# Performance work log

Measured on AMD Instinct MI355X. Metric: run time of the kernel, lower is better.

## Reference

```python
import jax, jax.numpy as jnp
import numpy as np

N_HEAD = 16
ROPE_BASE = 10000.0

def rotate_half(x):
    half = x.shape[-1] // 2
    return jnp.concatenate((-x[..., half:], x[..., :half]), axis=-1)

def rope_freqs(T, head_dim, dtype):
    inv_freq = 1.0 / (ROPE_BASE ** (jnp.arange(0, head_dim, 2, dtype=jnp.float32) / head_dim))
    t = jnp.arange(T, dtype=jnp.float32)
    freqs = t[:, None] * inv_freq[None, :]          # [T, head_dim//2]
    emb = jnp.concatenate((freqs, freqs), axis=-1)  # [T, head_dim]
    return emb.astype(dtype)

def setup_inputs() -> dict:
    key = jax.random.key(0)
    ks = jax.random.split(key, 9)
    B, T, C = 2, 2048, 1024
    s = 1.0 / np.sqrt(C)
    return {
        'x':  jax.random.normal(ks[0], (B, T, C), jnp.float32),
        'Wq': jax.random.normal(ks[1], (C, C), jnp.float32) * s,
        'bq': jnp.zeros((C,), jnp.float32),
        'Wk': jax.random.normal(ks[2], (C, C), jnp.float32) * s,
        'bk': jnp.zeros((C,), jnp.float32),
        'Wv': jax.random.normal(ks[3], (C, C), jnp.float32) * s,
        'bv': jnp.zeros((C,), jnp.float32),
        'Wp': jax.random.normal(ks[4], (C, C), jnp.float32) * s,
        'bp': jnp.zeros((C,), jnp.float32),
    }

def reference(x, Wq, bq, Wk, bk, Wv, bv, Wp, bp):
    B, T, C = x.shape
    H = N_HEAD
    D = C // H
    # torch Linear: y = x @ W.T + b
    def heads(y):
        return y.reshape(B, T, H, D).transpose(0, 2, 1, 3)  # [B,H,T,D]
    q = heads(x @ Wq.T + bq)
    k = heads(x @ Wk.T + bk)
    v = heads(x @ Wv.T + bv)
    # inline RoPE
    emb = rope_freqs(T, D, x.dtype)          # [T, D]
    cos, sin = jnp.cos(emb), jnp.sin(emb)
    q = q * cos + rotate_half(q) * sin
    k = k * cos + rotate_half(k) * sin
    # full T x T scores with causal masked softmax
    att = jnp.einsum('bhtd,bhsd->bhts', q, k) * (1.0 / jnp.sqrt(jnp.array(D, x.dtype)))
    causal = jnp.tril(jnp.ones((T, T), bool))
    att = jnp.where(causal[None, None], att, jnp.array(-jnp.inf, att.dtype))
    att = jax.nn.softmax(att, axis=-1)
    y = jnp.einsum('bhts,bhsd->bhtd', att, v)  # [B,H,T,D]
    y = y.transpose(0, 2, 1, 3).reshape(B, T, C)
    return y @ Wp.T + bp
```

## Files before the change

kernel.cpp:

```cpp
#include <hip/hip_runtime.h>
#include <hip/hip_bf16.h>
#include <stdint.h>

typedef unsigned short u16;
typedef __attribute__((ext_vector_type(8))) short bf16x8;
typedef __attribute__((ext_vector_type(4))) float f32x4;
typedef __attribute__((ext_vector_type(2))) unsigned int u32x2;

typedef const __attribute__((address_space(1))) unsigned int* gu32p;
typedef __attribute__((address_space(3))) unsigned int* lu32p;

__device__ __forceinline__ void gl_lds16(const u16* g, u16* l) {
  __builtin_amdgcn_global_load_lds((gu32p)(const void*)g, (lu32p)(void*)l, 16, 0, 0);
}

__device__ __forceinline__ u16 f2bf(float f) {
  union { float f; unsigned u; } v; v.f = f;
  unsigned r = v.u + 0x7fffu + ((v.u >> 16) & 1u);
  return (u16)(r >> 16);
}
__device__ __forceinline__ void st2bf(u16* p0, u16* p1, float a, float b) {
  union { __hip_bfloat162 h; u16 u[2]; } cv;
  cv.h = __float22bfloat162_rn(make_float2(a, b));
  *p0 = cv.u[0]; *p1 = cv.u[1];
}
__device__ __forceinline__ unsigned pk2bf(float a, float b) {
  union { __hip_bfloat162 h; unsigned u; } cv;
  cv.h = __float22bfloat162_rn(make_float2(a, b));
  return cv.u;
}

__global__ void convert_kernel(const float4* __restrict__ x, const float4* __restrict__ wq,
                               const float4* __restrict__ wk, const float4* __restrict__ wv,
                               const float4* __restrict__ wp,
                               u16* __restrict__ xb, u16* __restrict__ wqb, u16* __restrict__ wkb,
                               u16* __restrict__ wvb, u16* __restrict__ wpb,
                               float2* __restrict__ tab) {
  int i = blockIdx.x * 256 + threadIdx.x;
  const int NX = 1048576, NW = 262144, NCONV = NX + 4 * NW;
  if (i >= NCONV) {
    int j = i - NCONV;
    int d = j & 31, t = j >> 5;
    float ang = (float)t * expf(-0.28782313662425572f * (float)d);
    tab[j] = make_float2(cosf(ang), sinf(ang));
    return;
  }
  const float4* src; u16* dst; int off;
  if (i < NX)            { src = x;  dst = xb;  off = i; }
  else if (i < NX + NW)  { src = wq; dst = wqb; off = i - NX; }
  else if (i < NX + 2*NW){ src = wk; dst = wkb; off = i - NX - NW; }
  else if (i < NX + 3*NW){ src = wv; dst = wvb; off = i - NX - 2*NW; }
  else                   { src = wp; dst = wpb; off = i - NX - 3*NW; }
  float4 v = src[off];
  ushort4 ov = make_ushort4(f2bf(v.x), f2bf(v.y), f2bf(v.z), f2bf(v.w));
  *(ushort4*)&dst[off * 4] = ov;
}

template<int FUSE_ROPE, int OUT_BF16, int TRANS_V>
__global__ __launch_bounds__(256) void gemm_bt_kernel(
    const u16* __restrict__ A,
    const u16* __restrict__ B0, const u16* __restrict__ B1, const u16* __restrict__ B2,
    const float* __restrict__ bias0, const float* __restrict__ bias1, const float* __restrict__ bias2,
    void* out0, void* out1, void* out2, const float2* __restrict__ tab)
{
  __shared__ __align__(16) u16 As[2][4096];
  __shared__ __align__(16) u16 Bs[2][4096];
  const int z = blockIdx.z;
  const u16* Bw = (z == 0) ? B0 : (z == 1) ? B1 : B2;
  const float* bias = (z == 0) ? bias0 : (z == 1) ? bias1 : bias2;
  void* outv = (z == 0) ? out0 : (z == 1) ? out1 : out2;
  const int tid = threadIdx.x, lane = tid & 63, w = tid >> 6;
  const int wr = w >> 1, wc = w & 1;
  const int quad = lane >> 4, l15 = lane & 15;
  const int m0 = blockIdx.y * 128, n0 = blockIdx.x * 128;
  const int sr = lane >> 2, sc = (lane & 3) * 8;

  auto stg = [&](int kt, int bf) {
    const int k0 = kt * 32;
    #pragma unroll
    for (int p = 0; p < 2; p++) {
      gl_lds16(A  + (m0 + p*64 + w*16 + sr) * 1024 + k0 + sc, &As[bf][p*2048 + w*512]);
      gl_lds16(Bw + (n0 + p*64 + w*16 + sr) * 1024 + k0 + sc, &Bs[bf][p*2048 + w*512]);
    }
  };

  f32x4 acc[4][4] = {};
  stg(0, 0);
  for (int kt = 0; kt < 32; kt++) {
    __syncthreads();
    if (kt < 31) stg(kt + 1, (kt + 1) & 1);
    const int bf = kt & 1;
    bf16x8 af[4], bfr[4];
    #pragma unroll
    for (int mt = 0; mt < 4; mt++)
      af[mt] = *(const bf16x8*)&As[bf][(wr*64 + mt*16 + l15) * 32 + quad*8];
    #pragma unroll
    for (int nt = 0; nt < 4; nt++)
      bfr[nt] = *(const bf16x8*)&Bs[bf][(wc*64 + nt*16 + l15) * 32 + quad*8];
    #pragma unroll
    for (int mt = 0; mt < 4; mt++)
      #pragma unroll
      for (int nt = 0; nt < 4; nt++)
        acc[mt][nt] = __builtin_amdgcn_mfma_f32_16x16x32_bf16(af[mt], bfr[nt], acc[mt][nt], 0, 0, 0);
  }

  if (TRANS_V && z == 2) {
    const int bb = m0 >> 11, tg0 = (m0 & 2047) + wr*64 + quad*4;
    #pragma unroll
    for (int nt = 0; nt < 4; nt++) {
      const int c = n0 + wc*64 + nt*16 + l15;
      const float bv = bias[c];
      u16* vrow = (u16*)outv + (size_t)(bb*1024 + c) * 2048 + tg0;
      #pragma unroll
      for (int mt = 0; mt < 4; mt++) {
        ushort4 pk;
        pk.x = f2bf(acc[mt][nt][0] + bv); pk.y = f2bf(acc[mt][nt][1] + bv);
        pk.z = f2bf(acc[mt][nt][2] + bv); pk.w = f2bf(acc[mt][nt][3] + bv);
        *(ushort4*)&vrow[mt*16] = pk;
      }
    }
    return;
  }

  #pragma unroll
  for (int mt = 0; mt < 4; mt++) {
    #pragma unroll
    for (int r = 0; r < 4; r++) {
      const int row = m0 + wr*64 + mt*16 + quad*4 + r;
      float v[4];
      #pragma unroll
      for (int nt = 0; nt < 4; nt++)
        v[nt] = acc[mt][nt][r] + bias[n0 + wc*64 + nt*16 + l15];
      if (FUSE_ROPE && z < 2) {
        const int t = row & 2047;
        #pragma unroll
        for (int nt = 0; nt < 2; nt++) {
          const int d = nt*16 + l15;
          float2 cs = tab[t*32 + d];
          float x0 = v[nt], x1 = v[nt+2];
          v[nt]   = x0 * cs.x - x1 * cs.y;
          v[nt+2] = x1 * cs.x + x0 * cs.y;
        }
        if (z == 0) {
          const float SC = 0.18033688011112042f;
          #pragma unroll
          for (int nt = 0; nt < 4; nt++) v[nt] *= SC;
        }
      }
      #pragma unroll
      for (int nt = 0; nt < 4; nt++) {
        const int col = n0 + wc*64 + nt*16 + l15;
        if (OUT_BF16) ((u16*)outv)[row * 1024 + col] = f2bf(v[nt]);
        else          ((float*)outv)[row * 1024 + col] = v[nt];
      }
    }
  }
}

__global__ __launch_bounds__(256) void attn_kernel(
    const u16* __restrict__ qg, const u16* __restrict__ kg,
    const u16* __restrict__ vtg, u16* __restrict__ yg)
{
  __shared__ __align__(16) u16 K_lds[2][128 * 64];
  __shared__ __align__(16) u16 V_lds[2][64 * 128];
  const int x = blockIdx.x;
  const int hh = blockIdx.y, b = blockIdx.z;
  const int qt = b ? x : (15 - x);
  const int tid = threadIdx.x, lane = tid & 63, w = tid >> 6;
  const int quad = lane >> 4, l15 = lane & 15;
  const int bh = b * (2048 * 1024) + hh * 64;
  const int vtb = (b * 16 + hh) * 131072;

  bf16x8 qf[2][2];
  #pragma unroll
  for (int rg = 0; rg < 2; rg++) {
    const int qrow = qt*128 + rg*64 + w*16 + l15;
    qf[rg][0] = *(const bf16x8*)&qg[bh + qrow*1024 + quad*8];
    qf[rg][1] = *(const bf16x8*)&qg[bh + qrow*1024 + 32 + quad*8];
  }
  f32x4 o[2][4] = {};
  f32x4 l5[2] = {};

  bf16x8 ones;
  #pragma unroll
  for (int i2 = 0; i2 < 8; i2++) ones[i2] = (short)0x3F80;

  auto do_stage = [&](int j, int bf) {
    #pragma unroll
    for (int p = 0; p < 4; p++) {
      const int seg = w*4 + p;
      const int r = seg*8 + (lane >> 3);
      const int g = (lane & 7) ^ (r & 7);
      gl_lds16(kg + bh + (j*128 + r) * 1024 + g*8, &K_lds[bf][seg*512]);
    }
    #pragma unroll
    for (int p = 0; p < 4; p++) {
      const int seg = w*4 + p;
      const int r = seg*4 + (lane >> 4);
      const int g = (lane & 15) ^ (r & 15);
      gl_lds16(vtg + vtb + r * 2048 + j*128 + g*8, &V_lds[bf][seg*512]);
    }
  };

  do_stage(0, 0);
  for (int j = 0; j <= qt; j++) {
    __syncthreads();
    if (j < qt) do_stage(j + 1, (j + 1) & 1);
    const int bf = j & 1;
    const bool diag = (j == qt);

    #pragma unroll
    for (int ss = 0; ss < 4; ss++) {
      f32x4 s[2][2];
      #pragma unroll
      for (int h = 0; h < 2; h++) {
        const int nt = ss*2 + h;
        const int krow = (nt*16 + l15) * 64;
        const int g0 = ((quad)     ^ (l15 & 7)) * 8;
        const int g1 = ((4 + quad) ^ (l15 & 7)) * 8;
        bf16x8 kf0 = *(const bf16x8*)&K_lds[bf][krow + g0];
        bf16x8 kf1 = *(const bf16x8*)&K_lds[bf][krow + g1];
        #pragma unroll
        for (int rg = 0; rg < 2; rg++) {
          f32x4 z = {};
          z = __builtin_amdgcn_mfma_f32_16x16x32_bf16(kf0, qf[rg][0], z, 0, 0, 0);
          z = __builtin_amdgcn_mfma_f32_16x16x32_bf16(kf1, qf[rg][1], z, 0, 0, 0);
          s[rg][h] = z;
        }
      }
      if (diag) {
        #pragma unroll
        for (int rg = 0; rg < 2; rg++) {
          const int qrow = rg*64 + w*16 + l15;
          #pragma unroll
          for (int h = 0; h < 2; h++)
            #pragma unroll
            for (int r = 0; r < 4; r++)
              if ((ss*2 + h)*16 + quad*4 + r > qrow) s[rg][h][r] = -1e30f;
        }
      }
      bf16x8 pa[2];
      #pragma unroll
      for (int rg = 0; rg < 2; rg++) {
        float a0 = __builtin_amdgcn_exp2f(s[rg][0][0]), a1 = __builtin_amdgcn_exp2f(s[rg][0][1]);
        float a2 = __builtin_amdgcn_exp2f(s[rg][0][2]), a3 = __builtin_amdgcn_exp2f(s[rg][0][3]);
        float b0 = __builtin_amdgcn_exp2f(s[rg][1][0]), b1 = __builtin_amdgcn_exp2f(s[rg][1][1]);
        float b2 = __builtin_amdgcn_exp2f(s[rg][1][2]), b3 = __builtin_amdgcn_exp2f(s[rg][1][3]);
        unsigned A01 = pk2bf(a0, a1), A23 = pk2bf(a2, a3);
        unsigned B01 = pk2bf(b0, b1), B23 = pk2bf(b2, b3);
        u32x2 t0 = __builtin_amdgcn_permlane32_swap(A01, B01, false, false);
        u32x2 w02 = __builtin_amdgcn_permlane16_swap(t0[0], t0[1], false, false);
        u32x2 t1 = __builtin_amdgcn_permlane32_swap(A23, B23, false, false);
        u32x2 w13 = __builtin_amdgcn_permlane16_swap(t1[0], t1[1], false, false);
        union { unsigned u[4]; bf16x8 v; } pk;
        pk.u[0] = w02[0]; pk.u[1] = w13[0]; pk.u[2] = w02[1]; pk.u[3] = w13[1];
        pa[rg] = pk.v;
      }
      l5[0] = __builtin_amdgcn_mfma_f32_16x16x32_bf16(pa[0], ones, l5[0], 0, 0, 0);
      l5[1] = __builtin_amdgcn_mfma_f32_16x16x32_bf16(pa[1], ones, l5[1], 0, 0, 0);
      #pragma unroll
      for (int dt = 0; dt < 4; dt++) {
        const int vg = ((ss*4 + quad) ^ l15) * 8;
        bf16x8 vf = *(const bf16x8*)&V_lds[bf][(dt*16 + l15)*128 + vg];
        o[0][dt] = __builtin_amdgcn_mfma_f32_16x16x32_bf16(pa[0], vf, o[0][dt], 0, 0, 0);
        o[1][dt] = __builtin_amdgcn_mfma_f32_16x16x32_bf16(pa[1], vf, o[1][dt], 0, 0, 0);
      }
    }
  }

  #pragma unroll
  for (int rg = 0; rg < 2; rg++)
    #pragma unroll
    for (int r = 0; r < 4; r++) {
      float inv = 1.0f / l5[rg][r];
      u16* yr = &yg[bh + (qt*128 + rg*64 + w*16 + quad*4 + r) * 1024 + l15];
      st2bf(yr,      yr + 16, o[rg][0][r] * inv, o[rg][1][r] * inv);
      st2bf(yr + 32, yr + 48, o[rg][2][r] * inv, o[rg][3][r] * inv);
    }
}

extern "C" void kernel_launch(void* const* d_in, const int* in_sizes, int n_in,
                              void* d_out, int out_size, void* d_ws, size_t ws_size,
                              hipStream_t stream) {
  const float* x  = (const float*)d_in[0];
  const float* Wq = (const float*)d_in[1];
  const float* bq = (const float*)d_in[2];
  const float* Wk = (const float*)d_in[3];
  const float* bk = (const float*)d_in[4];
  const float* Wv = (const float*)d_in[5];
  const float* bv = (const float*)d_in[6];
  const float* Wp = (const float*)d_in[7];
  const float* bp = (const float*)d_in[8];

  char* ws = (char*)d_ws;
  u16* xb  = (u16*)(ws);
  u16* wqb = (u16*)(ws + (8u  << 20));
  u16* wkb = (u16*)(ws + (10u << 20));
  u16* wvb = (u16*)(ws + (12u << 20));
  u16* wpb = (u16*)(ws + (14u << 20));
  u16* qb  = (u16*)(ws + (16u << 20));
  u16* kb  = (u16*)(ws + (24u << 20));
  u16* vtb = (u16*)(ws + (32u << 20));
  float2* tab = (float2*)(ws + (40u << 20));
  u16* yb = xb;

  convert_kernel<<<8448, 256, 0, stream>>>((const float4*)x, (const float4*)Wq, (const float4*)Wk,
                                           (const float4*)Wv, (const float4*)Wp,
                                           xb, wqb, wkb, wvb, wpb, tab);
  gemm_bt_kernel<1, 1, 1><<<dim3(8, 32, 3), 256, 0, stream>>>(xb, wqb, wkb, wvb, bq, bk, bv,
                                                              (void*)qb, (void*)kb, (void*)vtb, tab);
  attn_kernel<<<dim3(16, 16, 2), 256, 0, stream>>>(qb, kb, vtb, yb);
  gemm_bt_kernel<0, 0, 0><<<dim3(8, 32, 1), 256, 0, stream>>>(yb, wpb, wpb, wpb, bp, bp, bp,
                                                              (void*)d_out, (void*)d_out, (void*)d_out, tab);
}
```

Before: 197.5 us.

## Swizzle GEMM LDS layout, remap workgroups across XCDs, narrow output-projection tiles

Adds an XOR swizzle to the 16-byte chunk positions in the GEMM LDS staging and fragment reads, which is meant to cut LDS bank conflicts. Remaps workgroup IDs in both the GEMM and attention kernels so that consecutive IDs land in contiguous chunks per XCD, which should improve L2 locality. Templates the GEMM on BN and runs the output projection with 64-wide N tiles, doubling its grid to 512 blocks for better CU occupancy. This trades more A-tile reloads for more parallelism. The FUSE_ROPE path still pairs nt with nt+2, which assumes NT=4, but it is only instantiated with BN=128.

```diff
diff --git a/kernel.cpp b/kernel.cpp
--- a/kernel.cpp
+++ b/kernel.cpp
@@ -56,59 +56,69 @@
   *(ushort4*)&dst[off * 4] = ov;
 }
 
-template<int FUSE_ROPE, int OUT_BF16, int TRANS_V>
+template<int FUSE_ROPE, int OUT_BF16, int TRANS_V, int BN, int NZ>
 __global__ __launch_bounds__(256) void gemm_bt_kernel(
     const u16* __restrict__ A,
     const u16* __restrict__ B0, const u16* __restrict__ B1, const u16* __restrict__ B2,
     const float* __restrict__ bias0, const float* __restrict__ bias1, const float* __restrict__ bias2,
     void* out0, void* out1, void* out2, const float2* __restrict__ tab)
 {
+  const int NT = BN / 32;
   __shared__ __align__(16) u16 As[2][4096];
-  __shared__ __align__(16) u16 Bs[2][4096];
-  const int z = blockIdx.z;
+  __shared__ __align__(16) u16 Bs[2][BN * 32];
+
+  const int NXg = 1024 / BN, NYg = 32;
+  const int nwg = NXg * NYg * NZ;
+  const int wgid = blockIdx.x + NXg * (blockIdx.y + NYg * blockIdx.z);
+  const int swz = (wgid & 7) * (nwg >> 3) + (wgid >> 3);
+  const int bx = swz % NXg, by = (swz / NXg) % NYg, z = swz / (NXg * NYg);
+
   const u16* Bw = (z == 0) ? B0 : (z == 1) ? B1 : B2;
   const float* bias = (z == 0) ? bias0 : (z == 1) ? bias1 : bias2;
   void* outv = (z == 0) ? out0 : (z == 1) ? out1 : out2;
   const int tid = threadIdx.x, lane = tid & 63, w = tid >> 6;
   const int wr = w >> 1, wc = w & 1;
   const int quad = lane >> 4, l15 = lane & 15;
-  const int m0 = blockIdx.y * 128, n0 = blockIdx.x * 128;
-  const int sr = lane >> 2, sc = (lane & 3) * 8;
+  const int m0 = by * 128, n0 = bx * BN;
+  const int sr = lane >> 2;
+  const int sg = ((lane & 3) ^ ((lane >> 3) & 3)) * 8;
+  const int rg4 = (l15 >> 1) & 3;
 
   auto stg = [&](int kt, int bf) {
     const int k0 = kt * 32;
     #pragma unroll
-    for (int p = 0; p < 2; p++) {
-      gl_lds16(A  + (m0 + p*64 + w*16 + sr) * 1024 + k0 + sc, &As[bf][p*2048 + w*512]);
-      gl_lds16(Bw + (n0 + p*64 + w*16 + sr) * 1024 + k0 + sc, &Bs[bf][p*2048 + w*512]);
-    }
+    for (int p = 0; p < 2; p++)
+      gl_lds16(A  + (m0 + p*64 + w*16 + sr) * 1024 + k0 + sg, &As[bf][p*2048 + w*512]);
+    #pragma unroll
+    for (int p = 0; p < BN/64; p++)
+      gl_lds16(Bw + (n0 + p*64 + w*16 + sr) * 1024 + k0 + sg, &Bs[bf][p*2048 + w*512]);
   };
 
-  f32x4 acc[4][4] = {};
+  f32x4 acc[4][NT] = {};
   stg(0, 0);
   for (int kt = 0; kt < 32; kt++) {
     __syncthreads();
     if (kt < 31) stg(kt + 1, (kt + 1) & 1);
     const int bf = kt & 1;
-    bf16x8 af[4], bfr[4];
+    bf16x8 af[4], bfr[NT];
     #pragma unroll
     for (int mt = 0; mt < 4; mt++)
-      af[mt] = *(const bf16x8*)&As[bf][(wr*64 + mt*16 + l15) * 32 + quad*8];
-    #pragma unroll
-    for (int nt = 0; nt < 4; nt++)
-      bfr[nt] = *(const bf16x8*)&Bs[bf][(wc*64 + nt*16 + l15) * 32 + quad*8];
+      af[mt] = *(const bf16x8*)&As[bf][(wr*64 + mt*16 + l15) * 32 + (quad ^ rg4) * 8];
+    #pragma unroll
+    for (int nt = 0; nt < NT; nt++)
+      bfr[nt] = *(const bf16x8*)&Bs[bf][(wc*(BN/2) + nt*16 + l15) * 32 + (quad ^ rg4) * 8];
     #pragma unroll
     for (int mt = 0; mt < 4; mt++)
       #pragma unroll
-      for (int nt = 0; nt < 4; nt++)
+      for (int nt = 0; nt < NT; nt++)
         acc[mt][nt] = __builtin_amdgcn_mfma_f32_16x16x32_bf16(af[mt], bfr[nt], acc[mt][nt], 0, 0, 0);
   }
 
   if (TRANS_V && z == 2) {
     const int bb = m0 >> 11, tg0 = (m0 & 2047) + wr*64 + quad*4;
     #pragma unroll
-    for (int nt = 0; nt < 4; nt++) {
-      const int c = n0 + wc*64 + nt*16 + l15;
+    for (int nt = 0; nt < NT; nt++) {
+      const int c = n0 + wc*(BN/2) + nt*16 + l15;
       const float bv = bias[c];
       u16* vrow = (u16*)outv + (size_t)(bb*1024 + c) * 2048 + tg0;
       #pragma unroll
@@ -127,10 +137,10 @@
     #pragma unroll
     for (int r = 0; r < 4; r++) {
       const int row = m0 + wr*64 + mt*16 + quad*4 + r;
-      float v[4];
-      #pragma unroll
-      for (int nt = 0; nt < 4; nt++)
-        v[nt] = acc[mt][nt][r] + bias[n0 + wc*64 + nt*16 + l15];
+      float v[NT];
+      #pragma unroll
+      for (int nt = 0; nt < NT; nt++)
+        v[nt] = acc[mt][nt][r] + bias[n0 + wc*(BN/2) + nt*16 + l15];
       if (FUSE_ROPE && z < 2) {
         const int t = row & 2047;
         #pragma unroll
@@ -144,12 +154,12 @@
         if (z == 0) {
           const float SC = 0.18033688011112042f;
           #pragma unroll
-          for (int nt = 0; nt < 4; nt++) v[nt] *= SC;
+          for (int nt = 0; nt < NT; nt++) v[nt] *= SC;
         }
       }
       #pragma unroll
-      for (int nt = 0; nt < 4; nt++) {
-        const int col = n0 + wc*64 + nt*16 + l15;
+      for (int nt = 0; nt < NT; nt++) {
+        const int col = n0 + wc*(BN/2) + nt*16 + l15;
         if (OUT_BF16) ((u16*)outv)[row * 1024 + col] = f2bf(v[nt]);
         else          ((float*)outv)[row * 1024 + col] = v[nt];
       }
@@ -163,8 +173,9 @@
 {
   __shared__ __align__(16) u16 K_lds[2][128 * 64];
   __shared__ __align__(16) u16 V_lds[2][64 * 128];
-  const int x = blockIdx.x;
-  const int hh = blockIdx.y, b = blockIdx.z;
+  const int wgid = blockIdx.x + 16 * (blockIdx.y + 16 * blockIdx.z);
+  const int swz = (wgid & 7) * 64 + (wgid >> 3);
+  const int x = swz & 15, hh = (swz >> 4) & 15, b = swz >> 8;
   const int qt = b ? x : (15 - x);
   const int tid = threadIdx.x, lane = tid & 63, w = tid >> 6;
   const int quad = lane >> 4, l15 = lane & 15;
@@ -307,9 +318,9 @@
   convert_kernel<<<8448, 256, 0, stream>>>((const float4*)x, (const float4*)Wq, (const float4*)Wk,
                                            (const float4*)Wv, (const float4*)Wp,
                                            xb, wqb, wkb, wvb, wpb, tab);
-  gemm_bt_kernel<1, 1, 1><<<dim3(8, 32, 3), 256, 0, stream>>>(xb, wqb, wkb, wvb, bq, bk, bv,
-                                                              (void*)qb, (void*)kb, (void*)vtb, tab);
+  gemm_bt_kernel<1, 1, 1, 128, 3><<<dim3(8, 32, 3), 256, 0, stream>>>(
+      xb, wqb, wkb, wvb, bq, bk, bv, (void*)qb, (void*)kb, (void*)vtb, tab);
   attn_kernel<<<dim3(16, 16, 2), 256, 0, stream>>>(qb, kb, vtb, yb);
-  gemm_bt_kernel<0, 0, 0><<<dim3(8, 32, 1), 256, 0, stream>>>(yb, wpb, wpb, wpb, bp, bp, bp,
-                                                              (void*)d_out, (void*)d_out, (void*)d_out, tab);
-}
+  gemm_bt_kernel<0, 0, 0, 64, 1><<<dim3(16, 32, 1), 256, 0, stream>>>(
+      yb, wpb, wpb, wpb, bp, bp, bp, (void*)d_out, (void*)d_out, (void*)d_out, tab);
+}
```

Measured after the change: 204.6 us. 3.6% more time.
